# Kernel optimization log

Measured on AMD Instinct MI355X. Metric: run time of the kernel, lower is better.

The kernel has to match this reference:

```python
import jax, jax.numpy as jnp
import numpy as np
import math

N_HEAD = 8

def setup_inputs() -> dict:
    key = jax.random.key(0)
    ks = jax.random.split(key, 5)
    B, T, D = 1, 4096, 512
    x = jax.random.normal(ks[0], (B, T, D), dtype=jnp.float32)
    s = 0.02
    Wq = jax.random.normal(ks[1], (D, D), dtype=jnp.float32) * s
    Wk = jax.random.normal(ks[2], (D, D), dtype=jnp.float32) * s
    Wv = jax.random.normal(ks[3], (D, D), dtype=jnp.float32) * s
    Wo = jax.random.normal(ks[4], (D, D), dtype=jnp.float32) * s
    return {"x": x, "Wq": Wq, "Wk": Wk, "Wv": Wv, "Wo": Wo, "window": 64}

def reference(x, Wq, Wk, Wv, Wo, window):
    # SparseAttention with attend_fn = causal sliding window of size `window`.
    # key_indices[q] = [max(0, q-window+1) .. q]
    B, T, D = x.shape
    H = N_HEAD
    Dh = D // H
    scale = math.sqrt(Dh)
    # torch Linear(bias=False): y = x @ W.T
    Q = (x @ Wq.T).reshape(B, T, H, Dh)
    K = (x @ Wk.T).reshape(B, T, H, Dh)
    V = (x @ Wv.T).reshape(B, T, H, Dh)
    # per-query gather indices [T, w] with validity mask (honors sparsity;
    # never materializes a [T, T] score matrix)
    offs = jnp.arange(window) - (window - 1)          # [-w+1 .. 0]
    idx = jnp.arange(T)[:, None] + offs[None, :]       # [T, w]
    valid = idx >= 0                                   # [T, w]
    idx_c = jnp.clip(idx, 0, T - 1)
    Kg = K[:, idx_c]                                   # [B, T, w, H, Dh]
    Vg = V[:, idx_c]                                   # [B, T, w, H, Dh]
    scores = jnp.einsum('bthd,btwhd->bhtw', Q, Kg) / scale
    scores = jnp.where(valid[None, None, :, :], scores, jnp.finfo(scores.dtype).min)
    attn = jax.nn.softmax(scores, axis=-1)             # dropout=0.0 (eval)
    out = jnp.einsum('bhtw,btwhd->bthd', attn, Vg).reshape(B, T, D)
    return out @ Wo.T
```

## Files before the change

### kernel.cpp

```cpp
#include <hip/hip_runtime.h>
#include <hip/hip_bf16.h>
#include <math.h>


typedef __attribute__((ext_vector_type(8))) short bf16frag;
typedef __attribute__((ext_vector_type(4))) float f32x4;
typedef __attribute__((ext_vector_type(8))) unsigned short u16x8;

#if defined(__has_builtin)
#if __has_builtin(__builtin_amdgcn_global_load_lds)
#define HAVE_GLOAD_LDS 1
#endif
#endif

__device__ inline void gload16(const void* g, void* l, int lane) {
#ifdef HAVE_GLOAD_LDS
    __builtin_amdgcn_global_load_lds(
        (const __attribute__((address_space(1))) void*)g,
        (__attribute__((address_space(3))) void*)l, 16, 0, 0);
#else
    *(bf16frag*)((char*)l + lane * 16) = *(const bf16frag*)g;
#endif
}

__device__ inline unsigned short bf16_rne(float f) {
    unsigned int u = __float_as_uint(f);
    unsigned int r = u + 0x7fffu + ((u >> 16) & 1u);
    return (unsigned short)(r >> 16);
}

__device__ inline void split_val(float f, unsigned short& h, unsigned short& l) {
    h = bf16_rne(f);
    float hf = __uint_as_float(((unsigned int)h) << 16);
    float lf = f - hf;
    l = bf16_rne(lf);
}

__global__ __launch_bounds__(256) void split5(
    const float* __restrict__ x, const float* __restrict__ wq, const float* __restrict__ wk,
    const float* __restrict__ wv, const float* __restrict__ wo,
    unsigned short* xh, unsigned short* xl, unsigned short* qh, unsigned short* ql,
    unsigned short* kh, unsigned short* kl, unsigned short* vh, unsigned short* vl,
    unsigned short* oh, unsigned short* ol, int nx, int nw)
{
    const float* src; unsigned short *H, *L; int n;
    switch (blockIdx.z) {
        case 0: src = x;  H = xh; L = xl; n = nx; break;
        case 1: src = wq; H = qh; L = ql; n = nw; break;
        case 2: src = wk; H = kh; L = kl; n = nw; break;
        case 3: src = wv; H = vh; L = vl; n = nw; break;
        default: src = wo; H = oh; L = ol; n = nw; break;
    }
    int stride = gridDim.x * blockDim.x * 4;
    for (int i = (blockIdx.x * blockDim.x + threadIdx.x) * 4; i < n; i += stride) {
        float4 f = *(const float4*)(src + i);
        ushort4 h4, l4;
        split_val(f.x, h4.x, l4.x);
        split_val(f.y, h4.y, l4.y);
        split_val(f.z, h4.z, l4.z);
        split_val(f.w, h4.w, l4.w);
        *(ushort4*)(H + i) = h4;
        *(ushort4*)(L + i) = l4;
    }
}

__global__ __launch_bounds__(256) void zero_pad(
    unsigned short* __restrict__ VTH, unsigned short* __restrict__ VTL, int vtw)
{
    int i = blockIdx.x * blockDim.x + threadIdx.x;
    if (i < 512 * 63) {
        int r = i / 63, c = i % 63;
        VTH[(size_t)r * vtw + c] = 0;
        VTL[(size_t)r * vtw + c] = 0;
    }
}

__global__ __launch_bounds__(256) void gemm_qkvt(
    const unsigned short* __restrict__ xh, const unsigned short* __restrict__ xl,
    const unsigned short* __restrict__ wqh, const unsigned short* __restrict__ wql,
    const unsigned short* __restrict__ wkh, const unsigned short* __restrict__ wkl,
    const unsigned short* __restrict__ wvh, const unsigned short* __restrict__ wvl,
    unsigned short* __restrict__ QHo, unsigned short* __restrict__ QLo,
    unsigned short* __restrict__ KHo, unsigned short* __restrict__ KLo,
    unsigned short* __restrict__ VTH, unsigned short* __restrict__ VTL,
    int T, int vtw)
{
    constexpr int ABYTES = 128 * 128;
    __shared__ unsigned char lds[2][(128 + 64) * 128];

    const int tid  = threadIdx.x;
    const int wid  = tid >> 6;
    const int lane = tid & 63;
    const int wr = wid >> 1, wc = wid & 1;

    const int NQK = 8 * (T / 128);
    const int id  = blockIdx.x;
    const unsigned short *Ah, *Al, *Bh, *Bl;
    unsigned short *OH_, *OL_;
    int m0, n0;
    bool vt;
    if (id < 2 * NQK) {
        vt = false;
        const int zq  = id / NQK;
        const int rem = id % NQK;
        n0 = (rem & 7) * 64;
        m0 = (rem >> 3) * 128;
        Ah = xh; Al = xl;
        Bh = zq ? wkh : wqh;  Bl = zq ? wkl : wql;
        OH_ = zq ? KHo : QHo; OL_ = zq ? KLo : QLo;
    } else {
        vt = true;
        const int rem = id - 2 * NQK;
        const int nx  = T / 64;
        n0 = (rem % nx) * 64;
        m0 = (rem / nx) * 128;
        Ah = wvh; Al = wvl;
        Bh = xh;  Bl = xl;
        OH_ = VTH; OL_ = VTL;
    }

    f32x4 acc[4][2];
    #pragma unroll
    for (int i = 0; i < 4; ++i) {
        acc[i][0] = (f32x4){0.f, 0.f, 0.f, 0.f};
        acc[i][1] = (f32x4){0.f, 0.f, 0.f, 0.f};
    }

    auto stage = [&](int buf, int ks) {
        const int rg = ks >> 3;
        const int k0 = (ks & 7) << 6;
        const unsigned short* As = (rg < 2) ? Ah : Al;
        const unsigned short* Bs = (rg == 1) ? Bl : Bh;
        #pragma unroll
        for (int j = 0; j < 6; ++j) {
            const int o  = (wid * 6 + j) << 10;
            const int li = o + lane * 16;
            const void* g;
            if (li < ABYTES) {
                const int r  = li >> 7;
                const int kb = (li & 127) ^ ((r & 7) << 4);
                g = As + (size_t)(m0 + r) * 512 + k0 + (kb >> 1);
            } else {
                const int lb = li - ABYTES;
                const int r  = lb >> 7;
                const int kb = (lb & 127) ^ ((r & 7) << 4);
                g = Bs + (size_t)(n0 + r) * 512 + k0 + (kb >> 1);
            }
            gload16(g, &lds[buf][o], lane);
        }
    };

    stage(0, 0);
    __syncthreads();
    int cur = 0;
    for (int ks = 0; ks < 24; ++ks) {
        if (ks < 23) stage(cur ^ 1, ks + 1);
        #pragma unroll
        for (int ksub = 0; ksub < 2; ++ksub) {
            const int kbb = (ksub << 6) + ((lane >> 4) << 4);
            bf16frag af[4], bf[2];
            #pragma unroll
            for (int mt = 0; mt < 4; ++mt) {
                const int r = wr * 64 + mt * 16 + (lane & 15);
                af[mt] = *(const bf16frag*)(&lds[cur][0] + r * 128 + (kbb ^ ((r & 7) << 4)));
            }
            #pragma unroll
            for (int nt = 0; nt < 2; ++nt) {
                const int r = wc * 32 + nt * 16 + (lane & 15);
                bf[nt] = *(const bf16frag*)(&lds[cur][0] + ABYTES + r * 128 + (kbb ^ ((r & 7) << 4)));
            }
            #pragma unroll
            for (int mt = 0; mt < 4; ++mt)
                #pragma unroll
                for (int nt = 0; nt < 2; ++nt)
                    acc[mt][nt] = __builtin_amdgcn_mfma_f32_16x16x32_bf16(
                        af[mt], bf[nt], acc[mt][nt], 0, 0, 0);
        }
        __syncthreads();
        cur ^= 1;
    }

    const int rbase = (lane >> 4) * 4;
    #pragma unroll
    for (int mt = 0; mt < 4; ++mt)
        #pragma unroll
        for (int nt = 0; nt < 2; ++nt) {
            const int col = n0 + wc * 32 + nt * 16 + (lane & 15);
            #pragma unroll
            for (int j = 0; j < 4; ++j) {
                const int row = m0 + wr * 64 + mt * 16 + rbase + j;
                unsigned short hh, ll;
                split_val(acc[mt][nt][j], hh, ll);
                if (!vt) {
                    OH_[(size_t)row * 512 + col] = hh;
                    OL_[(size_t)row * 512 + col] = ll;
                } else {
                    OH_[(size_t)row * vtw + 63 + col] = hh;
                    OL_[(size_t)row * vtw + 63 + col] = ll;
                }
            }
        }
}

__global__ __launch_bounds__(256) void gemm_out(
    const unsigned short* __restrict__ Ah, const unsigned short* __restrict__ Al,
    const unsigned short* __restrict__ Wh, const unsigned short* __restrict__ Wl,
    float* __restrict__ C)
{
    constexpr int ABYTES = 64 * 128;
    __shared__ unsigned char lds[2][(64 + 64) * 128];

    const int tid  = threadIdx.x;
    const int wid  = tid >> 6;
    const int lane = tid & 63;
    const int wr = wid >> 1, wc = wid & 1;
    const int m0 = blockIdx.y * 64;
    const int n0 = blockIdx.x * 64;

    f32x4 acc[2][2];
    #pragma unroll
    for (int i = 0; i < 2; ++i) {
        acc[i][0] = (f32x4){0.f, 0.f, 0.f, 0.f};
        acc[i][1] = (f32x4){0.f, 0.f, 0.f, 0.f};
    }

    auto stage = [&](int buf, int ks) {
        const int rg = ks >> 3;
        const int k0 = (ks & 7) << 6;
        const unsigned short* As = (rg < 2) ? Ah : Al;
        const unsigned short* Bs = (rg == 1) ? Wl : Wh;
        #pragma unroll
        for (int j = 0; j < 4; ++j) {
            const int o  = (wid * 4 + j) << 10;
            const int li = o + lane * 16;
            const void* g;
            if (li < ABYTES) {
                const int r  = li >> 7;
                const int kb = (li & 127) ^ ((r & 7) << 4);
                g = As + (size_t)(m0 + r) * 512 + k0 + (kb >> 1);
            } else {
                const int lb = li - ABYTES;
                const int r  = lb >> 7;
                const int kb = (lb & 127) ^ ((r & 7) << 4);
                g = Bs + (size_t)(n0 + r) * 512 + k0 + (kb >> 1);
            }
            gload16(g, &lds[buf][o], lane);
        }
    };

    stage(0, 0);
    __syncthreads();
    int cur = 0;
    for (int ks = 0; ks < 24; ++ks) {
        if (ks < 23) stage(cur ^ 1, ks + 1);
        #pragma unroll
        for (int ksub = 0; ksub < 2; ++ksub) {
            const int kbb = (ksub << 6) + ((lane >> 4) << 4);
            bf16frag af[2], bf[2];
            #pragma unroll
            for (int mt = 0; mt < 2; ++mt) {
                const int r = wr * 32 + mt * 16 + (lane & 15);
                af[mt] = *(const bf16frag*)(&lds[cur][0] + r * 128 + (kbb ^ ((r & 7) << 4)));
            }
            #pragma unroll
            for (int nt = 0; nt < 2; ++nt) {
                const int r = wc * 32 + nt * 16 + (lane & 15);
                bf[nt] = *(const bf16frag*)(&lds[cur][0] + ABYTES + r * 128 + (kbb ^ ((r & 7) << 4)));
            }
            #pragma unroll
            for (int mt = 0; mt < 2; ++mt)
                #pragma unroll
                for (int nt = 0; nt < 2; ++nt)
                    acc[mt][nt] = __builtin_amdgcn_mfma_f32_16x16x32_bf16(
                        af[mt], bf[nt], acc[mt][nt], 0, 0, 0);
        }
        __syncthreads();
        cur ^= 1;
    }

    const int rbase = (lane >> 4) * 4;
    #pragma unroll
    for (int mt = 0; mt < 2; ++mt)
        #pragma unroll
        for (int nt = 0; nt < 2; ++nt) {
            const int col = n0 + wc * 32 + nt * 16 + (lane & 15);
            #pragma unroll
            for (int j = 0; j < 4; ++j) {
                const int row = m0 + wr * 32 + mt * 16 + rbase + j;
                C[(size_t)row * 512 + col] = acc[mt][nt][j];
            }
        }
}

__global__ __launch_bounds__(128) void swattn5(
    const unsigned short* __restrict__ QH, const unsigned short* __restrict__ QL,
    const unsigned short* __restrict__ KH, const unsigned short* __restrict__ KL,
    const unsigned short* __restrict__ VTH, const unsigned short* __restrict__ VTL,
    unsigned short* __restrict__ OH, unsigned short* __restrict__ OL, int T)
{
    __shared__ unsigned short KsH[96 * 88], KsL[96 * 88];
    __shared__ unsigned short VtH[64 * 104], VtL[64 * 104];
    __shared__ unsigned short PsH[32 * 104], PsL[32 * 104];

    const int h   = blockIdx.x & 7;
    const int t0  = (blockIdx.x >> 3) * 32;
    const int kt0 = t0 - 63;
    const int tid = threadIdx.x;
    const int vtw = T + 64;

    {
        const int c = tid & 7;
        for (int r = tid >> 3; r < 96; r += 16) {
            const int kt = kt0 + r;
            u16x8 kh = {0,0,0,0,0,0,0,0}, kl = {0,0,0,0,0,0,0,0};
            if (kt >= 0 && r < 95) {
                const size_t off = (size_t)kt * 512 + h * 64 + c * 8;
                kh = *(const u16x8*)(KH + off);
                kl = *(const u16x8*)(KL + off);
            }
            *(u16x8*)&KsH[r * 88 + c * 8] = kh;
            *(u16x8*)&KsL[r * 88 + c * 8] = kl;
        }
    }
    for (int i = tid; i < 64 * 12; i += 128) {
        const int d = i / 12, c = i % 12;
        const size_t off = (size_t)(h * 64 + d) * vtw + t0 + c * 8;
        *(u16x8*)&VtH[d * 104 + c * 8] = *(const u16x8*)(VTH + off);
        *(u16x8*)&VtL[d * 104 + c * 8] = *(const u16x8*)(VTL + off);
    }
    __syncthreads();

    const int wid  = tid >> 6;
    const int lane = tid & 63;
    const int lr = lane & 15;
    const int lg = lane >> 4;

    bf16frag qfh[2], qfl[2];
    {
        const size_t base = (size_t)(t0 + wid * 16 + lr) * 512 + h * 64 + lg * 8;
        qfh[0] = *(const bf16frag*)(QH + base);
        qfh[1] = *(const bf16frag*)(QH + base + 32);
        qfl[0] = *(const bf16frag*)(QL + base);
        qfl[1] = *(const bf16frag*)(QL + base + 32);
    }

    f32x4 s[6];
    #pragma unroll
    for (int wt = 0; wt < 6; ++wt) s[wt] = (f32x4){0.f, 0.f, 0.f, 0.f};
    #pragma unroll
    for (int ksub = 0; ksub < 2; ++ksub) {
        #pragma unroll
        for (int wt = 0; wt < 6; ++wt) {
            const int a = (wt * 16 + lr) * 88 + lg * 8 + ksub * 32;
            bf16frag akh = *(const bf16frag*)&KsH[a];
            bf16frag akl = *(const bf16frag*)&KsL[a];
            s[wt] = __builtin_amdgcn_mfma_f32_16x16x32_bf16(akh, qfh[ksub], s[wt], 0, 0, 0);
            s[wt] = __builtin_amdgcn_mfma_f32_16x16x32_bf16(akh, qfl[ksub], s[wt], 0, 0, 0);
            s[wt] = __builtin_amdgcn_mfma_f32_16x16x32_bf16(akl, qfh[ksub], s[wt], 0, 0, 0);
        }
    }

    const int q_local = wid * 16 + lr;
    float sc[6][4];
    float mx = -3e38f;
    #pragma unroll
    for (int wt = 0; wt < 6; ++wt)
        #pragma unroll
        for (int j = 0; j < 4; ++j) {
            const int w = wt * 16 + lg * 4 + j;
            const bool valid = (w >= q_local) && (w <= q_local + 63) && (kt0 + w >= 0);
            sc[wt][j] = valid ? s[wt][j] * 0.125f : -3e38f;
            mx = fmaxf(mx, sc[wt][j]);
        }
    mx = fmaxf(mx, __shfl_xor(mx, 16));
    mx = fmaxf(mx, __shfl_xor(mx, 32));
    float sum = 0.f;
    #pragma unroll
    for (int wt = 0; wt < 6; ++wt)
        #pragma unroll
        for (int j = 0; j < 4; ++j) {
            sc[wt][j] = __expf(sc[wt][j] - mx);
            sum += sc[wt][j];
        }
    sum += __shfl_xor(sum, 16);
    sum += __shfl_xor(sum, 32);
    const float inv = 1.f / sum;

    #pragma unroll
    for (int wt = 0; wt < 6; ++wt) {
        ushort4 ph, pl;
        unsigned short hh, ll;
        split_val(sc[wt][0] * inv, hh, ll); ph.x = hh; pl.x = ll;
        split_val(sc[wt][1] * inv, hh, ll); ph.y = hh; pl.y = ll;
        split_val(sc[wt][2] * inv, hh, ll); ph.z = hh; pl.z = ll;
        split_val(sc[wt][3] * inv, hh, ll); ph.w = hh; pl.w = ll;
        const int col = wt * 16 + lg * 4;
        *(ushort4*)&PsH[q_local * 104 + col] = ph;
        *(ushort4*)&PsL[q_local * 104 + col] = pl;
    }

    f32x4 oa[4];
    #pragma unroll
    for (int dt = 0; dt < 4; ++dt) oa[dt] = (f32x4){0.f, 0.f, 0.f, 0.f};
    #pragma unroll
    for (int ks = 0; ks < 3; ++ks) {
        const int ka = lg * 8 + ks * 32;
        bf16frag pah = *(const bf16frag*)&PsH[(wid * 16 + lr) * 104 + ka];
        bf16frag pal = *(const bf16frag*)&PsL[(wid * 16 + lr) * 104 + ka];
        #pragma unroll
        for (int dt = 0; dt < 4; ++dt) {
            const int a = (dt * 16 + lr) * 104 + ka;
            bf16frag bvh = *(const bf16frag*)&VtH[a];
            bf16frag bvl = *(const bf16frag*)&VtL[a];
            oa[dt] = __builtin_amdgcn_mfma_f32_16x16x32_bf16(pah, bvh, oa[dt], 0, 0, 0);
            oa[dt] = __builtin_amdgcn_mfma_f32_16x16x32_bf16(pal, bvh, oa[dt], 0, 0, 0);
            oa[dt] = __builtin_amdgcn_mfma_f32_16x16x32_bf16(pah, bvl, oa[dt], 0, 0, 0);
        }
    }

    #pragma unroll
    for (int dt = 0; dt < 4; ++dt) {
        const int d = dt * 16 + lr;
        #pragma unroll
        for (int j = 0; j < 4; ++j) {
            const int t = t0 + wid * 16 + lg * 4 + j;
            unsigned short hh, ll;
            split_val(oa[dt][j], hh, ll);
            const size_t oi = (size_t)t * 512 + h * 64 + d;
            OH[oi] = hh;
            OL[oi] = ll;
        }
    }
}

extern "C" void kernel_launch(void* const* d_in, const int* in_sizes, int n_in,
                              void* d_out, int out_size, void* d_ws, size_t ws_size,
                              hipStream_t stream) {
    const float* x  = (const float*)d_in[0];
    const float* Wq = (const float*)d_in[1];
    const float* Wk = (const float*)d_in[2];
    const float* Wv = (const float*)d_in[3];
    const float* Wo = (const float*)d_in[4];
    float* out = (float*)d_out;

    const int D = 512;
    const int T = in_sizes[0] / D;
    const size_t tdf = (size_t)T * D;
    const size_t wsz = (size_t)D * D;
    const int vtw = T + 64;
    const size_t vts = (size_t)D * vtw;

    unsigned short* qh  = (unsigned short*)d_ws;
    unsigned short* ql  = qh + tdf;
    unsigned short* kh  = ql + tdf;
    unsigned short* kl  = kh + tdf;
    unsigned short* vth = kl + tdf;
    unsigned short* vtl = vth + vts;
    unsigned short* abh = vtl + vts;
    unsigned short* abl = abh + tdf;
    unsigned short* xh  = abl + tdf;
    unsigned short* xl  = xh + tdf;
    unsigned short* wqh = xl + tdf;
    unsigned short* wql = wqh + wsz;
    unsigned short* wkh = wql + wsz;
    unsigned short* wkl = wkh + wsz;
    unsigned short* wvh = wkl + wsz;
    unsigned short* wvl = wvh + wsz;
    unsigned short* woh = wvl + wsz;
    unsigned short* wol = woh + wsz;

    dim3 blk(256);
    split5<<<dim3(256, 1, 5), blk, 0, stream>>>(
        x, Wq, Wk, Wv, Wo, xh, xl, wqh, wql, wkh, wkl, wvh, wvl, woh, wol,
        (int)tdf, (int)wsz);

    zero_pad<<<dim3((512 * 63 + 255) / 256), blk, 0, stream>>>(vth, vtl, vtw);

    const int NQK = 8 * (T / 128);
    const int NVT = (T / 64) * (D / 128);
    gemm_qkvt<<<dim3(2 * NQK + NVT), blk, 0, stream>>>(
        xh, xl, wqh, wql, wkh, wkl, wvh, wvl,
        qh, ql, kh, kl, vth, vtl, T, vtw);

    swattn5<<<dim3(8 * T / 32), dim3(128), 0, stream>>>(
        qh, ql, kh, kl, vth, vtl, abh, abl, T);

    gemm_out<<<dim3(D / 64, T / 64), blk, 0, stream>>>(
        abh, abl, woh, wol, out);
}
```

Before: 140.4 us.

## Fold zero-pad into QKV GEMM, remap blocks per XCD, and relax load waits

Removes the separate zero_pad launch and has the V^T blocks with n0==0 zero their padding columns inside gemm_qkvt. Both GEMMs remap block indices so that consecutive logical tiles land on the same XCD, aiming for better L2 reuse. The double-buffered loops replace __syncthreads with explicit partial vmcnt waits plus raw barriers, so the prefetch for the next stage can stay in flight while the current tile is computed. The hand-counted waits rely on the compiler issuing exactly the expected number of memory operations, and the remap assumes the grid size divides by 8.

```diff
diff --git a/kernel.cpp b/kernel.cpp
--- a/kernel.cpp
+++ b/kernel.cpp
@@ -64,17 +64,6 @@
     }
 }
 
-__global__ __launch_bounds__(256) void zero_pad(
-    unsigned short* __restrict__ VTH, unsigned short* __restrict__ VTL, int vtw)
-{
-    int i = blockIdx.x * blockDim.x + threadIdx.x;
-    if (i < 512 * 63) {
-        int r = i / 63, c = i % 63;
-        VTH[(size_t)r * vtw + c] = 0;
-        VTL[(size_t)r * vtw + c] = 0;
-    }
-}
-
 __global__ __launch_bounds__(256) void gemm_qkvt(
     const unsigned short* __restrict__ xh, const unsigned short* __restrict__ xl,
     const unsigned short* __restrict__ wqh, const unsigned short* __restrict__ wql,
@@ -93,8 +82,10 @@
     const int lane = tid & 63;
     const int wr = wid >> 1, wc = wid & 1;
 
+    const int chunk = gridDim.x >> 3;
+    const int id = (blockIdx.x & 7) * chunk + (blockIdx.x >> 3);
+
     const int NQK = 8 * (T / 128);
-    const int id  = blockIdx.x;
     const unsigned short *Ah, *Al, *Bh, *Bl;
     unsigned short *OH_, *OL_;
     int m0, n0;
@@ -117,6 +108,13 @@
         Ah = wvh; Al = wvl;
         Bh = xh;  Bl = xl;
         OH_ = VTH; OL_ = VTL;
+        if (n0 == 0) {
+            for (int i = tid; i < 128 * 63; i += 256) {
+                const int r = i / 63, c = i % 63;
+                VTH[(size_t)(m0 + r) * vtw + c] = 0;
+                VTL[(size_t)(m0 + r) * vtw + c] = 0;
+            }
+        }
     }
 
     f32x4 acc[4][2];
@@ -151,10 +149,17 @@
     };
 
     stage(0, 0);
-    __syncthreads();
+    asm volatile("s_waitcnt vmcnt(0)" ::: "memory");
+    __builtin_amdgcn_s_barrier();
     int cur = 0;
     for (int ks = 0; ks < 24; ++ks) {
-        if (ks < 23) stage(cur ^ 1, ks + 1);
+        if (ks < 23) {
+            stage(cur ^ 1, ks + 1);
+            asm volatile("s_waitcnt vmcnt(6)" ::: "memory");
+        } else {
+            asm volatile("s_waitcnt vmcnt(0)" ::: "memory");
+        }
+        __builtin_amdgcn_s_barrier();
         #pragma unroll
         for (int ksub = 0; ksub < 2; ++ksub) {
             const int kbb = (ksub << 6) + ((lane >> 4) << 4);
@@ -176,7 +181,7 @@
                     acc[mt][nt] = __builtin_amdgcn_mfma_f32_16x16x32_bf16(
                         af[mt], bf[nt], acc[mt][nt], 0, 0, 0);
         }
-        __syncthreads();
+        __builtin_amdgcn_s_barrier();
         cur ^= 1;
     }
 
@@ -205,7 +210,7 @@
 __global__ __launch_bounds__(256) void gemm_out(
     const unsigned short* __restrict__ Ah, const unsigned short* __restrict__ Al,
     const unsigned short* __restrict__ Wh, const unsigned short* __restrict__ Wl,
-    float* __restrict__ C)
+    float* __restrict__ C, int T)
 {
     constexpr int ABYTES = 64 * 128;
     __shared__ unsigned char lds[2][(64 + 64) * 128];
@@ -214,8 +219,11 @@
     const int wid  = tid >> 6;
     const int lane = tid & 63;
     const int wr = wid >> 1, wc = wid & 1;
-    const int m0 = blockIdx.y * 64;
-    const int n0 = blockIdx.x * 64;
+
+    const int chunk = gridDim.x >> 3;
+    const int b = (blockIdx.x & 7) * chunk + (blockIdx.x >> 3);
+    const int n0 = (b & 7) * 64;
+    const int m0 = (b >> 3) * 64;
 
     f32x4 acc[2][2];
     #pragma unroll
@@ -249,10 +257,17 @@
     };
 
     stage(0, 0);
-    __syncthreads();
+    asm volatile("s_waitcnt vmcnt(0)" ::: "memory");
+    __builtin_amdgcn_s_barrier();
     int cur = 0;
     for (int ks = 0; ks < 24; ++ks) {
-        if (ks < 23) stage(cur ^ 1, ks + 1);
+        if (ks < 23) {
+            stage(cur ^ 1, ks + 1);
+            asm volatile("s_waitcnt vmcnt(4)" ::: "memory");
+        } else {
+            asm volatile("s_waitcnt vmcnt(0)" ::: "memory");
+        }
+        __builtin_amdgcn_s_barrier();
         #pragma unroll
         for (int ksub = 0; ksub < 2; ++ksub) {
             const int kbb = (ksub << 6) + ((lane >> 4) << 4);
@@ -274,7 +289,7 @@
                     acc[mt][nt] = __builtin_amdgcn_mfma_f32_16x16x32_bf16(
                         af[mt], bf[nt], acc[mt][nt], 0, 0, 0);
         }
-        __syncthreads();
+        __builtin_amdgcn_s_barrier();
         cur ^= 1;
     }
 
@@ -474,8 +489,6 @@
         x, Wq, Wk, Wv, Wo, xh, xl, wqh, wql, wkh, wkl, wvh, wvl, woh, wol,
         (int)tdf, (int)wsz);
 
-    zero_pad<<<dim3((512 * 63 + 255) / 256), blk, 0, stream>>>(vth, vtl, vtw);
-
     const int NQK = 8 * (T / 128);
     const int NVT = (T / 64) * (D / 128);
     gemm_qkvt<<<dim3(2 * NQK + NVT), blk, 0, stream>>>(
@@ -485,6 +498,6 @@
     swattn5<<<dim3(8 * T / 32), dim3(128), 0, stream>>>(
         qh, ql, kh, kl, vth, vtl, abh, abl, T);
 
-    gemm_out<<<dim3(D / 64, T / 64), blk, 0, stream>>>(
-        abh, abl, woh, wol, out);
-}
+    gemm_out<<<dim3((T / 64) * (D / 64)), blk, 0, stream>>>(
+        abh, abl, woh, wol, out, T);
+}
```

Measured after the change: 134.4 us. -4.2%, faster.
